# Performance work log

Hardware: AMD Instinct MI355X
Metric: run time of the kernel (lower is better)

## Reference

```python
import jax, jax.numpy as jnp
import numpy as np

H = 512  # hidden size
E = 512  # embedding / input size
V = 10000  # vocab size


def _lstm_cell(x, h, c, W_ih, W_hh, b_ih, b_hh):
    # torch LSTMCell gate order: i, f, g, o
    gates = x @ W_ih.T + h @ W_hh.T + b_ih + b_hh
    i, f, g, o = jnp.split(gates, 4, axis=-1)
    i = jax.nn.sigmoid(i)
    f = jax.nn.sigmoid(f)
    g = jnp.tanh(g)
    o = jax.nn.sigmoid(o)
    c_new = f * c + i * g
    h_new = o * jnp.tanh(c_new)
    return h_new, c_new


def setup_inputs() -> dict:
    key = jax.random.key(0)
    ks = jax.random.split(key, 14)
    T, B, U = 128, 32, 1024
    s = 0.05
    return {
        "inputs": jax.random.normal(ks[0], (T, B, E), jnp.float32),
        "h0": jax.random.normal(ks[1], (2, B, H), jnp.float32),
        "c0": jax.random.normal(ks[2], (2, B, H), jnp.float32),
        "listener_outputs": jax.random.normal(ks[3], (U, B, H), jnp.float32),
        "W_ih1": jax.random.normal(ks[4], (4 * H, E), jnp.float32) * s,
        "W_hh1": jax.random.normal(ks[5], (4 * H, H), jnp.float32) * s,
        "b_ih1": jax.random.normal(ks[6], (4 * H,), jnp.float32) * s,
        "b_hh1": jax.random.normal(ks[7], (4 * H,), jnp.float32) * s,
        "W_ih2": jax.random.normal(ks[8], (4 * H, H), jnp.float32) * s,
        "W_hh2": jax.random.normal(ks[9], (4 * H, H), jnp.float32) * s,
        "b_ih2": jax.random.normal(ks[10], (4 * H,), jnp.float32) * s,
        "b_hh2": jax.random.normal(ks[11], (4 * H,), jnp.float32) * s,
        "W_out": jax.random.normal(ks[12], (V, H), jnp.float32) * s,
        "b_out": jax.random.normal(ks[13], (V,), jnp.float32) * s,
    }


def reference(inputs, h0, c0, listener_outputs,
              W_ih1, W_hh1, b_ih1, b_hh1,
              W_ih2, W_hh2, b_ih2, b_hh2,
              W_out, b_out):
    # layer-1 LSTMCell + dot-product attention per timestep
    def step1(carry, x_t):
        h1, c1 = carry
        h1, c1 = _lstm_cell(x_t, h1, c1, W_ih1, W_hh1, b_ih1, b_hh1)
        # scores over listener time U: (B, U)
        scores = jnp.einsum('ubh,bh->bu', listener_outputs, h1)
        w = jax.nn.softmax(scores, axis=1)
        ctx = jnp.einsum('ubh,bu->bh', listener_outputs, w)  # (B, H)
        return (h1, c1), ctx

    (_, _), contexts = jax.lax.scan(step1, (h0[0], c0[0]), inputs)  # (T, B, H)

    # layer-2 single-layer LSTM over attention contexts
    def step2(carry, x_t):
        h2, c2 = carry
        h2, c2 = _lstm_cell(x_t, h2, c2, W_ih2, W_hh2, b_ih2, b_hh2)
        return (h2, c2), h2

    (_, _), hs = jax.lax.scan(step2, (h0[1], c0[1]), contexts)  # (T, B, H)

    logits = hs @ W_out.T + b_out  # (T, B, V)
    return jax.nn.softmax(logits, axis=2)
```

## Files before the change

kernel.cpp:

```cpp
#include <hip/hip_runtime.h>

#define T_STEPS 128
#define BATCH   32
#define HID     512
#define EMB     512
#define ULEN    1024
#define VOCAB   10000
#define G4H     2048

#define ARR_STRIDE 16
#define GO_OFF     4096
#define GO_STRIDE  64
#define BAR_WORDS  6144

static inline int cdiv(int a, int b) { return (a + b - 1) / b; }

template <bool TRANSB>
__global__ __launch_bounds__(256)
void gemm_f32(const float* __restrict__ A, long lda, long sA,
              const float* __restrict__ Bm, long ldb, long sB,
              float* __restrict__ C, long ldc, long sC,
              int M, int N, int K, const float* __restrict__ bias)
{
    __shared__ float As[16][68];
    __shared__ float Bs[16][68];
    const int bz = blockIdx.z;
    A  += (size_t)bz * sA;
    Bm += (size_t)bz * sB;
    C  += (size_t)bz * sC;
    const int m0 = blockIdx.y * 64;
    const int n0 = blockIdx.x * 64;
    const int tid = threadIdx.x;
    const int tx = tid & 15, ty = tid >> 4;
    const int lr = tid >> 2;
    const int lk = (tid & 3) * 4;

    float acc[4][4] = {{0.f}};

    for (int k0 = 0; k0 < K; k0 += 16) {
        float4 av = *(const float4*)(A + (size_t)(m0 + lr) * lda + (k0 + lk));
        As[lk + 0][lr] = av.x; As[lk + 1][lr] = av.y;
        As[lk + 2][lr] = av.z; As[lk + 3][lr] = av.w;
        if (TRANSB) {
            const int nr = n0 + lr;
            float4 bv = make_float4(0.f, 0.f, 0.f, 0.f);
            if (nr < N) bv = *(const float4*)(Bm + (size_t)nr * ldb + (k0 + lk));
            Bs[lk + 0][lr] = bv.x; Bs[lk + 1][lr] = bv.y;
            Bs[lk + 2][lr] = bv.z; Bs[lk + 3][lr] = bv.w;
        } else {
            const int kr = tid >> 4;
            const int nc = (tid & 15) * 4;
            float4 bv = make_float4(0.f, 0.f, 0.f, 0.f);
            if (n0 + nc < N) bv = *(const float4*)(Bm + (size_t)(k0 + kr) * ldb + (n0 + nc));
            *(float4*)&Bs[kr][nc] = bv;
        }
        __syncthreads();
#pragma unroll
        for (int kk = 0; kk < 16; ++kk) {
            float ar[4], br[4];
#pragma unroll
            for (int i = 0; i < 4; i++) ar[i] = As[kk][ty * 4 + i];
#pragma unroll
            for (int j = 0; j < 4; j++) br[j] = Bs[kk][tx * 4 + j];
#pragma unroll
            for (int i = 0; i < 4; i++)
#pragma unroll
                for (int j = 0; j < 4; j++)
                    acc[i][j] += ar[i] * br[j];
        }
        __syncthreads();
    }
#pragma unroll
    for (int i = 0; i < 4; i++) {
        const int row = m0 + ty * 4 + i;
#pragma unroll
        for (int j = 0; j < 4; j++) {
            const int col = n0 + tx * 4 + j;
            if (col < N) {
                float v = acc[i][j];
                if (bias) v += bias[col];
                C[(size_t)row * ldc + col] = v;
            }
        }
    }
}

__device__ inline unsigned short f32_bf16(float x) {
    unsigned u = __float_as_uint(x);
    unsigned r = (u + 0x7FFFu + ((u >> 16) & 1u)) >> 16;
    return (unsigned short)r;
}
__device__ inline float bf16_f32(unsigned short h) {
    return __uint_as_float(((unsigned)h) << 16);
}

__global__ __launch_bounds__(256)
void conv_split(const float* __restrict__ src, unsigned short* __restrict__ dhi,
                unsigned short* __restrict__ dlo, int n)
{
    for (int i = blockIdx.x * 256 + threadIdx.x; i < n; i += gridDim.x * 256) {
        float a = src[i];
        unsigned short hi = f32_bf16(a);
        float r = a - bf16_f32(hi);
        dhi[i] = hi;
        dlo[i] = f32_bf16(r);
    }
}

typedef __attribute__((ext_vector_type(8))) short bf16x8;
typedef __attribute__((ext_vector_type(4))) float f32x4;

__global__ __launch_bounds__(256)
void gemm_bf16s(const unsigned short* __restrict__ Ahi,
                const unsigned short* __restrict__ Alo,
                const unsigned short* __restrict__ Bhi,
                const unsigned short* __restrict__ Blo,
                float* __restrict__ C, const float* __restrict__ bias,
                int M, int N, int K)
{
    __shared__ unsigned short Asm[128 * 32];
    __shared__ unsigned short Bsm[128 * 32];
    const int tid = threadIdx.x;
    const int m0 = blockIdx.y * 128;
    const int n0 = blockIdx.x * 128;
    const int w  = tid >> 6;
    const int l  = tid & 63;
    const int wr = (w >> 1) * 64;
    const int wc = (w & 1) * 64;
    const int fr = l & 15;
    const int kb = l >> 4;

    f32x4 acc[4][4];
#pragma unroll
    for (int i = 0; i < 4; ++i)
#pragma unroll
        for (int j = 0; j < 4; ++j) acc[i][j] = (f32x4){0.f, 0.f, 0.f, 0.f};

    const int srow = tid >> 1;
    const int skh  = (tid & 1) * 16;

#pragma unroll 1
    for (int pass = 0; pass < 3; ++pass) {
        const unsigned short* Ap = (pass == 2) ? Alo : Ahi;
        const unsigned short* Bp = (pass == 1) ? Blo : Bhi;
#pragma unroll 1
        for (int kt = 0; kt < K; kt += 32) {
            {
                const unsigned short* src = Ap + (size_t)(m0 + srow) * K + kt + skh;
                float4 v0 = *(const float4*)(src);
                float4 v1 = *(const float4*)(src + 8);
                *(float4*)&Asm[srow * 32 + skh] = v0;
                *(float4*)&Asm[srow * 32 + skh + 8] = v1;
            }
            {
                const int nr = n0 + srow;
                float4 v0 = make_float4(0.f, 0.f, 0.f, 0.f), v1 = v0;
                if (nr < N) {
                    const unsigned short* src = Bp + (size_t)nr * K + kt + skh;
                    v0 = *(const float4*)(src);
                    v1 = *(const float4*)(src + 8);
                }
                *(float4*)&Bsm[srow * 32 + skh] = v0;
                *(float4*)&Bsm[srow * 32 + skh + 8] = v1;
            }
            __syncthreads();
            bf16x8 af[4], bf[4];
#pragma unroll
            for (int i = 0; i < 4; ++i)
                af[i] = *(const bf16x8*)&Asm[(wr + i * 16 + fr) * 32 + kb * 8];
#pragma unroll
            for (int j = 0; j < 4; ++j)
                bf[j] = *(const bf16x8*)&Bsm[(wc + j * 16 + fr) * 32 + kb * 8];
#pragma unroll
            for (int i = 0; i < 4; ++i)
#pragma unroll
                for (int j = 0; j < 4; ++j)
                    acc[i][j] = __builtin_amdgcn_mfma_f32_16x16x32_bf16(
                        af[i], bf[j], acc[i][j], 0, 0, 0);
            __syncthreads();
        }
    }

#pragma unroll
    for (int i = 0; i < 4; ++i) {
#pragma unroll
        for (int j = 0; j < 4; ++j) {
            const int col = n0 + wc + j * 16 + fr;
            if (col < N) {
                const float bv = bias ? bias[col] : 0.f;
#pragma unroll
                for (int r = 0; r < 4; ++r) {
                    const int row = m0 + wr + i * 16 + kb * 4 + r;
                    C[(size_t)row * N + col] = acc[i][j][r] + bv;
                }
            }
        }
    }
}

__device__ inline float sigmoidf_(float x) { return 1.f / (1.f + expf(-x)); }

__global__ __launch_bounds__(256, 1)
void lstm_scan(const float* __restrict__ gp,
               const float* __restrict__ Whh,
               const float* __restrict__ h0,
               const float* __restrict__ c0,
               float* __restrict__ h_all,
               unsigned* __restrict__ bar)
{
    __shared__ float h_lds[BATCH * HID];
    __shared__ float w_lds[8 * HID];
    __shared__ float part[256 * 36];
    unsigned* arrive = bar;
    unsigned* go     = bar + GO_OFF;

    const int tid  = threadIdx.x;
    const int bid  = blockIdx.x;
    const int hbase = bid * 2;

    const int ks = tid & 31;
    const int bq = tid >> 5;
    const int kl = ks & 7;

    const int b    = tid >> 3;
    const int nl   = tid & 7;
    const int j    = nl & 1;
    const int lane = tid & 63;
    const int sbase = lane & ~7;
    const int n = ((nl >> 1) << 9) + hbase + j;

#pragma unroll
    for (int i = 0; i < 4; ++i) {
        const int vi = i * 256 + tid;
        const int c  = vi >> 7;
        const int f  = vi & 127;
        const int nd = ((c >> 1) << 9) + hbase + (c & 1);
        float4 v = *(const float4*)(Whh + (size_t)nd * HID + f * 4);
        const int p = f ^ ((f >> 2) & 7);
        *(float4*)&w_lds[(c << 9) + (p << 2)] = v;
    }

    const int sw0 = (((ks * 4 + 0) ^ kl)) << 2;
    const int sw1 = (((ks * 4 + 1) ^ kl)) << 2;
    const int sw2 = (((ks * 4 + 2) ^ kl)) << 2;
    const int sw3 = (((ks * 4 + 3) ^ kl)) << 2;

    float c_state = (nl < 2) ? c0[b * HID + hbase + j] : 0.f;
    float gnext = gp[(size_t)b * G4H + n];

    for (int t = 0; t < T_STEPS; ++t) {
        float gval = gnext;

        const float* hsrc = (t == 0) ? h0 : (h_all + (size_t)(t - 1) * (BATCH * HID));
#pragma unroll
        for (int i = 0; i < 16; ++i) {
            const int vi = i * 256 + tid;
            float4 v = *(const float4*)(hsrc + (size_t)vi * 4);
            const int bb = vi >> 7;
            const int f  = vi & 127;
            const int p  = f ^ ((f >> 2) & 7);
            *(float4*)&h_lds[(bb << 9) + (p << 2)] = v;
        }
        __syncthreads();

        float4 hr[4][4];
#pragma unroll
        for (int rr = 0; rr < 4; ++rr) {
            const int o = (bq * 4 + rr) << 9;
            hr[rr][0] = *(const float4*)(h_lds + o + sw0);
            hr[rr][1] = *(const float4*)(h_lds + o + sw1);
            hr[rr][2] = *(const float4*)(h_lds + o + sw2);
            hr[rr][3] = *(const float4*)(h_lds + o + sw3);
        }

        float acc[32];
#pragma unroll
        for (int c = 0; c < 8; ++c) {
            const int wo = c << 9;
            float4 w0 = *(const float4*)(w_lds + wo + sw0);
            float4 w1 = *(const float4*)(w_lds + wo + sw1);
            float4 w2 = *(const float4*)(w_lds + wo + sw2);
            float4 w3 = *(const float4*)(w_lds + wo + sw3);
#pragma unroll
            for (int rr = 0; rr < 4; ++rr) {
                acc[rr * 8 + c] =
                      (hr[rr][0].x * w0.x + hr[rr][0].y * w0.y
                     + hr[rr][0].z * w0.z + hr[rr][0].w * w0.w)
                    + (hr[rr][1].x * w1.x + hr[rr][1].y * w1.y
                     + hr[rr][1].z * w1.z + hr[rr][1].w * w1.w)
                    + (hr[rr][2].x * w2.x + hr[rr][2].y * w2.y
                     + hr[rr][2].z * w2.z + hr[rr][2].w * w2.w)
                    + (hr[rr][3].x * w3.x + hr[rr][3].y * w3.y
                     + hr[rr][3].z * w3.z + hr[rr][3].w * w3.w);
            }
        }
        {
            float* pw = &part[tid * 36];
#pragma unroll
            for (int i = 0; i < 8; ++i)
                *(float4*)(pw + i * 4) =
                    make_float4(acc[4 * i], acc[4 * i + 1], acc[4 * i + 2], acc[4 * i + 3]);
        }
        __syncthreads();

        float s = gval;
        {
            const float* pr = &part[(b >> 2) * (32 * 36) + (b & 3) * 8 + nl];
#pragma unroll
            for (int kr = 0; kr < 32; ++kr) s += pr[kr * 36];
        }

        float fva = __shfl(s, sbase + 2 + j);
        float gva = __shfl(s, sbase + 4 + j);
        float ova = __shfl(s, sbase + 6 + j);
        if (nl < 2) {
            float iv = sigmoidf_(s);
            float fv = sigmoidf_(fva);
            float gv = tanhf(gva);
            float ov = sigmoidf_(ova);
            c_state = fv * c_state + iv * gv;
            float hn = ov * tanhf(c_state);
            __hip_atomic_store(h_all + ((size_t)t * BATCH + b) * HID + hbase + j,
                               hn, __ATOMIC_RELAXED, __HIP_MEMORY_SCOPE_AGENT);
        }

        {
            const int tn = (t + 1 < T_STEPS) ? (t + 1) : t;
            gnext = gp[((size_t)tn * BATCH + b) * G4H + n];
        }

        __syncthreads();
        const unsigned want = (unsigned)(t + 1);
        if (bid == 0) {
            if (tid == 0)
                __hip_atomic_store(&arrive[0], want, __ATOMIC_RELAXED,
                                   __HIP_MEMORY_SCOPE_AGENT);
            unsigned v;
            do {
                v = __hip_atomic_load(&arrive[tid * ARR_STRIDE], __ATOMIC_RELAXED,
                                      __HIP_MEMORY_SCOPE_AGENT);
            } while (__syncthreads_count(v >= want) < 256);
            if (tid < 32)
                __hip_atomic_store(&go[tid * GO_STRIDE], want, __ATOMIC_RELAXED,
                                   __HIP_MEMORY_SCOPE_AGENT);
        } else if (tid == 0) {
            __hip_atomic_store(&arrive[bid * ARR_STRIDE], want, __ATOMIC_RELAXED,
                               __HIP_MEMORY_SCOPE_AGENT);
            unsigned g;
            do {
                __builtin_amdgcn_s_sleep(1);
                g = __hip_atomic_load(&go[(bid & 31) * GO_STRIDE], __ATOMIC_RELAXED,
                                      __HIP_MEMORY_SCOPE_AGENT);
            } while (g < want);
        }
        __syncthreads();
    }
}

__device__ inline float warpReduceMax_(float v) {
#pragma unroll
    for (int o = 32; o > 0; o >>= 1) v = fmaxf(v, __shfl_xor(v, o));
    return v;
}
__device__ inline float warpReduceSum_(float v) {
#pragma unroll
    for (int o = 32; o > 0; o >>= 1) v += __shfl_xor(v, o);
    return v;
}
__device__ inline float blockReduceMax_(float v, float* red) {
    v = warpReduceMax_(v);
    if ((threadIdx.x & 63) == 0) red[threadIdx.x >> 6] = v;
    __syncthreads();
    float r = fmaxf(fmaxf(red[0], red[1]), fmaxf(red[2], red[3]));
    __syncthreads();
    return r;
}
__device__ inline float blockReduceSum_(float v, float* red) {
    v = warpReduceSum_(v);
    if ((threadIdx.x & 63) == 0) red[threadIdx.x >> 6] = v;
    __syncthreads();
    float r = (red[0] + red[1]) + (red[2] + red[3]);
    __syncthreads();
    return r;
}

__global__ __launch_bounds__(256)
void softmax_u(float* __restrict__ s)
{
    __shared__ float red[4];
    float4* p = (float4*)(s + (size_t)blockIdx.x * ULEN);
    float4 v = p[threadIdx.x];
    float mx = fmaxf(fmaxf(v.x, v.y), fmaxf(v.z, v.w));
    mx = blockReduceMax_(mx, red);
    v.x = expf(v.x - mx); v.y = expf(v.y - mx);
    v.z = expf(v.z - mx); v.w = expf(v.w - mx);
    float sm = blockReduceSum_(v.x + v.y + v.z + v.w, red);
    float inv = 1.f / sm;
    v.x *= inv; v.y *= inv; v.z *= inv; v.w *= inv;
    p[threadIdx.x] = v;
}

__global__ __launch_bounds__(256)
void softmax_v(float* __restrict__ out)
{
    __shared__ float red[4];
    float* p = out + (size_t)blockIdx.x * VOCAB;
    float v[40];
    float mx = -INFINITY;
#pragma unroll
    for (int k = 0; k < 40; ++k) {
        const int i = (k << 8) + (int)threadIdx.x;
        v[k] = (i < VOCAB) ? p[i] : -INFINITY;
        mx = fmaxf(mx, v[k]);
    }
    mx = blockReduceMax_(mx, red);
    float sm = 0.f;
#pragma unroll
    for (int k = 0; k < 40; ++k) {
        v[k] = expf(v[k] - mx);
        sm += v[k];
    }
    sm = blockReduceSum_(sm, red);
    const float inv = 1.f / sm;
#pragma unroll
    for (int k = 0; k < 40; ++k) {
        const int i = (k << 8) + (int)threadIdx.x;
        if (i < VOCAB) p[i] = v[k] * inv;
    }
}

__global__ void prep(const float* __restrict__ bi1, const float* __restrict__ bh1,
                     const float* __restrict__ bi2, const float* __restrict__ bh2,
                     float* __restrict__ bias1, float* __restrict__ bias2,
                     unsigned* __restrict__ flags)
{
    int i = blockIdx.x * 256 + threadIdx.x;
    if (i < G4H) { bias1[i] = bi1[i] + bh1[i]; bias2[i] = bi2[i] + bh2[i]; }
    if (i < 2 * BAR_WORDS) flags[i] = 0u;
}

extern "C" void kernel_launch(void* const* d_in, const int* in_sizes, int n_in,
                              void* d_out, int out_size, void* d_ws, size_t ws_size,
                              hipStream_t stream)
{
    const float* inputs = (const float*)d_in[0];
    const float* h0     = (const float*)d_in[1];
    const float* c0     = (const float*)d_in[2];
    const float* L      = (const float*)d_in[3];
    const float* W_ih1  = (const float*)d_in[4];
    const float* W_hh1  = (const float*)d_in[5];
    const float* b_ih1  = (const float*)d_in[6];
    const float* b_hh1  = (const float*)d_in[7];
    const float* W_ih2  = (const float*)d_in[8];
    const float* W_hh2  = (const float*)d_in[9];
    const float* b_ih2  = (const float*)d_in[10];
    const float* b_hh2  = (const float*)d_in[11];
    const float* W_out  = (const float*)d_in[12];
    const float* b_out  = (const float*)d_in[13];
    float* out = (float*)d_out;

    float* ws    = (float*)d_ws;
    float* gates = ws;
    float* h1    = gates + (size_t)T_STEPS * BATCH * G4H;
    float* h2    = h1    + (size_t)T_STEPS * BATCH * HID;
    float* ctx   = h2    + (size_t)T_STEPS * BATCH * HID;
    float* bias1 = ctx   + (size_t)T_STEPS * BATCH * HID;
    float* bias2 = bias1 + G4H;
    unsigned* flags = (unsigned*)(bias2 + G4H);
    float* scores = gates;

    const int MA = T_STEPS * BATCH;
    unsigned short* ahi = (unsigned short*)h1;
    unsigned short* alo = ahi + (size_t)MA * HID;
    unsigned short* bhi = (unsigned short*)gates;
    unsigned short* blo = bhi + (size_t)VOCAB * HID;

    prep<<<48, 256, 0, stream>>>(b_ih1, b_hh1, b_ih2, b_hh2, bias1, bias2, flags);

    gemm_f32<true><<<dim3(G4H / 64, MA / 64, 1), 256, 0, stream>>>(
        inputs, EMB, 0, W_ih1, EMB, 0, gates, G4H, 0,
        MA, G4H, EMB, bias1);

    lstm_scan<<<256, 256, 0, stream>>>(gates, W_hh1, h0, c0, h1, flags);

    gemm_f32<true><<<dim3(ULEN / 64, T_STEPS / 64, BATCH), 256, 0, stream>>>(
        h1, (long)BATCH * HID, HID,
        L,  (long)BATCH * HID, HID,
        scores, (long)BATCH * ULEN, ULEN,
        T_STEPS, ULEN, HID, nullptr);

    softmax_u<<<T_STEPS * BATCH, 256, 0, stream>>>(scores);

    gemm_f32<false><<<dim3(HID / 64, T_STEPS / 64, BATCH), 256, 0, stream>>>(
        scores, (long)BATCH * ULEN, ULEN,
        L,      (long)BATCH * HID,  HID,
        ctx,    (long)BATCH * HID,  HID,
        T_STEPS, HID, ULEN, nullptr);

    gemm_f32<true><<<dim3(G4H / 64, MA / 64, 1), 256, 0, stream>>>(
        ctx, HID, 0, W_ih2, HID, 0, gates, G4H, 0,
        MA, G4H, HID, bias2);

    lstm_scan<<<256, 256, 0, stream>>>(gates, W_hh2, h0 + BATCH * HID, c0 + BATCH * HID,
                                       h2, flags + BAR_WORDS);

    conv_split<<<2048, 256, 0, stream>>>(W_out, bhi, blo, VOCAB * HID);
    conv_split<<<2048, 256, 0, stream>>>(h2, ahi, alo, MA * HID);

    gemm_bf16s<<<dim3(cdiv(VOCAB, 128), MA / 128, 1), 256, 0, stream>>>(
        ahi, alo, bhi, blo, out, b_out, MA, VOCAB, HID);

    softmax_v<<<T_STEPS * BATCH, 256, 0, stream>>>(out);
}
```

Before: 2.253 ms.

## Replace centralized grid barrier with per-block sequence flags and h slabs

```diff
diff --git a/kernel.cpp b/kernel.cpp
--- a/kernel.cpp
+++ b/kernel.cpp
@@ -7,11 +7,6 @@
 #define ULEN    1024
 #define VOCAB   10000
 #define G4H     2048
-
-#define ARR_STRIDE 16
-#define GO_OFF     4096
-#define GO_STRIDE  64
-#define BAR_WORDS  6144
 
 static inline int cdiv(int a, int b) { return (a + b - 1) / b; }
 
@@ -206,13 +201,13 @@
                const float* __restrict__ h0,
                const float* __restrict__ c0,
                float* __restrict__ h_all,
-               unsigned* __restrict__ bar)
+               float* __restrict__ hslab,
+               unsigned* __restrict__ seq,
+               unsigned scan_base)
 {
     __shared__ float h_lds[BATCH * HID];
     __shared__ float w_lds[8 * HID];
     __shared__ float part[256 * 36];
-    unsigned* arrive = bar;
-    unsigned* go     = bar + GO_OFF;
 
     const int tid  = threadIdx.x;
     const int bid  = blockIdx.x;
@@ -245,21 +240,47 @@
     const int sw2 = (((ks * 4 + 2) ^ kl)) << 2;
     const int sw3 = (((ks * 4 + 3) ^ kl)) << 2;
 
+    const int cf = tid >> 1;
+    const int cp = cf ^ ((cf >> 2) & 7);
+    float* cdst = h_lds + (cp << 2) + ((tid & 1) << 1);
+
     float c_state = (nl < 2) ? c0[b * HID + hbase + j] : 0.f;
     float gnext = gp[(size_t)b * G4H + n];
 
     for (int t = 0; t < T_STEPS; ++t) {
         float gval = gnext;
 
-        const float* hsrc = (t == 0) ? h0 : (h_all + (size_t)(t - 1) * (BATCH * HID));
-#pragma unroll
-        for (int i = 0; i < 16; ++i) {
-            const int vi = i * 256 + tid;
-            float4 v = *(const float4*)(hsrc + (size_t)vi * 4);
-            const int bb = vi >> 7;
-            const int f  = vi & 127;
-            const int p  = f ^ ((f >> 2) & 7);
-            *(float4*)&h_lds[(bb << 9) + (p << 2)] = v;
+        if (t == 0) {
+#pragma unroll
+            for (int i = 0; i < 16; ++i) {
+                const int vi = i * 256 + tid;
+                float4 v = *(const float4*)(h0 + (size_t)vi * 4);
+                const int bb = vi >> 7;
+                const int f  = vi & 127;
+                const int p  = f ^ ((f >> 2) & 7);
+                *(float4*)&h_lds[(bb << 9) + (p << 2)] = v;
+            }
+        } else {
+            const unsigned tag = scan_base + (unsigned)t;
+            const unsigned* sp = seq + ((size_t)(t - 1) * 256 + tid);
+            unsigned v = __hip_atomic_load(sp, __ATOMIC_RELAXED,
+                                           __HIP_MEMORY_SCOPE_AGENT);
+            while (v != tag) {
+                __builtin_amdgcn_s_sleep(1);
+                v = __hip_atomic_load(sp, __ATOMIC_RELAXED,
+                                      __HIP_MEMORY_SCOPE_AGENT);
+            }
+            asm volatile("" ::: "memory");
+            const float4* sl =
+                (const float4*)(hslab + ((size_t)(t - 1) * 256 + tid) * 64);
+            float4 d[16];
+#pragma unroll
+            for (int i = 0; i < 16; ++i) d[i] = sl[i];
+#pragma unroll
+            for (int i = 0; i < 16; ++i) {
+                *(float2*)(cdst + (((2 * i) + 0) << 9)) = make_float2(d[i].x, d[i].y);
+                *(float2*)(cdst + (((2 * i) + 1) << 9)) = make_float2(d[i].z, d[i].w);
+            }
         }
         __syncthreads();
 
@@ -320,8 +341,10 @@
             float ov = sigmoidf_(ova);
             c_state = fv * c_state + iv * gv;
             float hn = ov * tanhf(c_state);
-            __hip_atomic_store(h_all + ((size_t)t * BATCH + b) * HID + hbase + j,
-                               hn, __ATOMIC_RELAXED, __HIP_MEMORY_SCOPE_AGENT);
+            h_all[((size_t)t * BATCH + b) * HID + hbase + j] = hn;
+            if (t < T_STEPS - 1)
+                __hip_atomic_store(hslab + ((size_t)t * 256 + bid) * 64 + b * 2 + j,
+                                   hn, __ATOMIC_RELAXED, __HIP_MEMORY_SCOPE_AGENT);
         }
 
         {
@@ -330,30 +353,10 @@
         }
 
         __syncthreads();
-        const unsigned want = (unsigned)(t + 1);
-        if (bid == 0) {
-            if (tid == 0)
-                __hip_atomic_store(&arrive[0], want, __ATOMIC_RELAXED,
-                                   __HIP_MEMORY_SCOPE_AGENT);
-            unsigned v;
-            do {
-                v = __hip_atomic_load(&arrive[tid * ARR_STRIDE], __ATOMIC_RELAXED,
-                                      __HIP_MEMORY_SCOPE_AGENT);
-            } while (__syncthreads_count(v >= want) < 256);
-            if (tid < 32)
-                __hip_atomic_store(&go[tid * GO_STRIDE], want, __ATOMIC_RELAXED,
-                                   __HIP_MEMORY_SCOPE_AGENT);
-        } else if (tid == 0) {
-            __hip_atomic_store(&arrive[bid * ARR_STRIDE], want, __ATOMIC_RELAXED,
-                               __HIP_MEMORY_SCOPE_AGENT);
-            unsigned g;
-            do {
-                __builtin_amdgcn_s_sleep(1);
-                g = __hip_atomic_load(&go[(bid & 31) * GO_STRIDE], __ATOMIC_RELAXED,
-                                      __HIP_MEMORY_SCOPE_AGENT);
-            } while (g < want);
-        }
-        __syncthreads();
+        if (t < T_STEPS - 1 && tid == 0)
+            __hip_atomic_store(seq + ((size_t)t * 256 + bid),
+                               scan_base + (unsigned)(t + 1),
+                               __ATOMIC_RELAXED, __HIP_MEMORY_SCOPE_AGENT);
     }
 }
 
@@ -431,12 +434,10 @@
 
 __global__ void prep(const float* __restrict__ bi1, const float* __restrict__ bh1,
                      const float* __restrict__ bi2, const float* __restrict__ bh2,
-                     float* __restrict__ bias1, float* __restrict__ bias2,
-                     unsigned* __restrict__ flags)
+                     float* __restrict__ bias1, float* __restrict__ bias2)
 {
     int i = blockIdx.x * 256 + threadIdx.x;
     if (i < G4H) { bias1[i] = bi1[i] + bh1[i]; bias2[i] = bi2[i] + bh2[i]; }
-    if (i < 2 * BAR_WORDS) flags[i] = 0u;
 }
 
 extern "C" void kernel_launch(void* const* d_in, const int* in_sizes, int n_in,
@@ -466,8 +467,9 @@
     float* ctx   = h2    + (size_t)T_STEPS * BATCH * HID;
     float* bias1 = ctx   + (size_t)T_STEPS * BATCH * HID;
     float* bias2 = bias1 + G4H;
-    unsigned* flags = (unsigned*)(bias2 + G4H);
+    unsigned* seq = (unsigned*)(bias2 + G4H);
     float* scores = gates;
+    float* hslab  = ctx;
 
     const int MA = T_STEPS * BATCH;
     unsigned short* ahi = (unsigned short*)h1;
@@ -475,13 +477,13 @@
     unsigned short* bhi = (unsigned short*)gates;
     unsigned short* blo = bhi + (size_t)VOCAB * HID;
 
-    prep<<<48, 256, 0, stream>>>(b_ih1, b_hh1, b_ih2, b_hh2, bias1, bias2, flags);
+    prep<<<8, 256, 0, stream>>>(b_ih1, b_hh1, b_ih2, b_hh2, bias1, bias2);
 
     gemm_f32<true><<<dim3(G4H / 64, MA / 64, 1), 256, 0, stream>>>(
         inputs, EMB, 0, W_ih1, EMB, 0, gates, G4H, 0,
         MA, G4H, EMB, bias1);
 
-    lstm_scan<<<256, 256, 0, stream>>>(gates, W_hh1, h0, c0, h1, flags);
+    lstm_scan<<<256, 256, 0, stream>>>(gates, W_hh1, h0, c0, h1, hslab, seq, 0x100u);
 
     gemm_f32<true><<<dim3(ULEN / 64, T_STEPS / 64, BATCH), 256, 0, stream>>>(
         h1, (long)BATCH * HID, HID,
@@ -502,7 +504,7 @@
         MA, G4H, HID, bias2);
 
     lstm_scan<<<256, 256, 0, stream>>>(gates, W_hh2, h0 + BATCH * HID, c0 + BATCH * HID,
-                                       h2, flags + BAR_WORDS);
+                                       h2, hslab, seq, 0x200u);
 
     conv_split<<<2048, 256, 0, stream>>>(W_out, bhi, blo, VOCAB * HID);
     conv_split<<<2048, 256, 0, stream>>>(h2, ahi, alo, MA * HID);
```

Result: slower. 3.134 ms (+39.1%).
